# Optimization experiments

Measured on AMD Instinct MI355X. Metric: run time of the kernel, lower is better.

## Reference

```python
import jax, jax.numpy as jnp
import numpy as np

N, F_IN, H, C, E = 20000, 512, 256, 40, 640000
TEMPERATURE = 1.0


def setup_inputs() -> dict:
    key = jax.random.key(0)
    k0, k1, k2, k3 = jax.random.split(key, 4)
    x = jax.random.normal(k0, (N, F_IN), dtype=jnp.float32)
    edge_index = jax.random.randint(k1, (2, E), 0, N, dtype=jnp.int32)
    W1 = jax.random.normal(k2, (F_IN, H), dtype=jnp.float32) / np.float32(np.sqrt(F_IN))
    b1 = jnp.zeros((H,), dtype=jnp.float32)
    W2 = jax.random.normal(k3, (H, C), dtype=jnp.float32) / np.float32(np.sqrt(H))
    b2 = jnp.zeros((C,), dtype=jnp.float32)
    return {"x": x, "edge_index": edge_index, "W1": W1, "b1": b1, "W2": W2, "b2": b2}


def _gcn_conv(x, W, b, src, dst, dinv):
    """GCNConv with added self-loops and symmetric normalization.
    out_i = sum_{j->i} d_i^{-1/2} d_j^{-1/2} (x_j W) + d_i^{-1} (x_i W) + b
    """
    h = x @ W                                         # [N, out]
    coef = dinv[src] * dinv[dst]                      # [E]
    msg = h[src] * coef[:, None]                      # [E, out] gathered messages
    agg = jax.ops.segment_sum(msg, dst, num_segments=x.shape[0])
    agg = agg + h * (dinv * dinv)[:, None]            # self-loop contribution
    return agg + b


def reference(x, edge_index, W1, b1, W2, b2):
    src, dst = edge_index[0], edge_index[1]
    n = x.shape[0]
    # degree including self-loop (PyG gcn_norm counts in-degree on dst)
    deg = jax.ops.segment_sum(jnp.ones(src.shape[0], x.dtype), dst, num_segments=n) + 1.0
    dinv = jax.lax.rsqrt(deg)
    h = jax.nn.relu(_gcn_conv(x, W1, b1, src, dst, dinv))
    # dropout is identity in eval mode (training=False)
    out = _gcn_conv(h, W2, b2, src, dst, dinv)
    return out / jnp.asarray(TEMPERATURE, dtype=out.dtype)
```

## Files before the change

kernel.cpp:

```cpp
#include <hip/hip_runtime.h>
#include <hip/hip_bf16.h>


#define N_NODES 20000
#define F_IN    512
#define H_DIM   256
#define C_DIM   40
#define C_PAD   64
#define E_EDGES 640000
#define BCAP    96
#define WB      576
#define FSH     8
#define FCH     320
#define FCE     2000
#define NSH     2500
#define POISON  0xAAAAAAAAu
#define FXSCALE 2048.f
#define INV_SCALE (1.f / 2048.f)

typedef __attribute__((ext_vector_type(8))) short short8;
typedef __attribute__((ext_vector_type(4))) float floatx4;

__device__ __forceinline__ unsigned short f2bf(float f) {
    unsigned int u = __float_as_uint(f);
    unsigned int r = (u + 0x7fffu + ((u >> 16) & 1u)) >> 16;
    return (unsigned short)r;
}
__device__ __forceinline__ float lo16(unsigned int u) { return __uint_as_float(u << 16); }
__device__ __forceinline__ float hi16(unsigned int u) { return __uint_as_float(u & 0xffff0000u); }
__device__ __forceinline__ unsigned int pack2(float a, float b) {
    return (unsigned int)f2bf(a) | ((unsigned int)f2bf(b) << 16);
}
__device__ __forceinline__ int degof(const int* cursor, int i) {
    return (int)((unsigned)cursor[i] - POISON);
}
#define ACC8F(A, v) do { \
    A[0] += lo16((v).x); A[1] += hi16((v).x); \
    A[2] += lo16((v).y); A[3] += hi16((v).y); \
    A[4] += lo16((v).z); A[5] += hi16((v).z); \
    A[6] += lo16((v).w); A[7] += hi16((v).w); } while (0)
#define ACC8W(A, v) do { \
    A[0] += (int)(short)((v).x & 0xffffu); A[1] += ((int)(v).x) >> 16; \
    A[2] += (int)(short)((v).y & 0xffffu); A[3] += ((int)(v).y) >> 16; \
    A[4] += (int)(short)((v).z & 0xffffu); A[5] += ((int)(v).z) >> 16; \
    A[6] += (int)(short)((v).w & 0xffffu); A[7] += ((int)(v).w) >> 16; } while (0)


__global__ __launch_bounds__(256) void fillwt_kernel(const int* __restrict__ src,
                                                     const int* __restrict__ dst,
                                                     int* __restrict__ cursor,
                                                     int* __restrict__ esrc,
                                                     const float* __restrict__ W1,
                                                     const float* __restrict__ W2,
                                                     unsigned short* __restrict__ w1t,
                                                     unsigned short* __restrict__ w2t,
                                                     short* __restrict__ h1w,
                                                     unsigned short* __restrict__ h2b) {
    const int b = blockIdx.x, t = threadIdx.x;
    if (b < FSH * FCH) {
        const int shard = b & 7;
        const int chunk = b >> 3;
        const int lo = shard * NSH;
        const int base = chunk * FCE;
#pragma unroll
        for (int it = 0; it < 8; ++it) {
            int o = it * 256 + t;
            if (o < FCE) {
                int e = base + o;
                int d = dst[e];
                if ((unsigned)(d - lo) < (unsigned)NSH) {
                    unsigned slot = (unsigned)atomicAdd(&cursor[d], 1) - POISON;
                    esrc[d * BCAP + slot] = src[e];
                }
            }
        }
    } else if (b < FSH * FCH + WB) {
        int idx = (b - FSH * FCH) * 256 + t;
        if (idx < F_IN * H_DIM) {
            int n = idx >> 9, k = idx & 511;
            w1t[idx] = f2bf(W1[k * H_DIM + n]);
        } else {
            int id2 = idx - F_IN * H_DIM;
            int n = id2 >> 8, k = id2 & 255;
            w2t[id2] = (n < C_DIM) ? f2bf(W2[k * C_DIM + n]) : (unsigned short)0;
        }
    } else {
        h1w[(size_t)N_NODES * H_DIM + t] = 0;
        if (t < C_PAD) h2b[(size_t)N_NODES * C_PAD + t] = 0;
    }
}


__global__ __launch_bounds__(256) void gemm1_kernel(const float* __restrict__ A,
                                                    const unsigned short* __restrict__ BT,
                                                    const int* __restrict__ cursor,
                                                    short* __restrict__ Cw) {
    __shared__ short As[64 * 40];
    __shared__ short Bs[128 * 40];
    const int b = blockIdx.x;
    const int tid = threadIdx.x;
    const int w = tid >> 6;
    const int lane = tid & 63;
    const int lq = lane >> 4;
    const int lm = lane & 15;
    const int row0 = (b >> 1) * 64;
    const int col0 = (b & 1) * 128;
    const int sr = tid >> 2;
    const int sc = (tid & 3) * 8;

    floatx4 acc[8];
#pragma unroll
    for (int t = 0; t < 8; ++t) acc[t] = (floatx4){0.f, 0.f, 0.f, 0.f};

    for (int k0 = 0; k0 < F_IN; k0 += 32) {
        {
            const int gr = row0 + sr;
            short8 av = (short8){0,0,0,0,0,0,0,0};
            if (gr < N_NODES) {
                const float* p = A + (size_t)gr * F_IN + k0 + sc;
                float4 a0 = *(const float4*)p;
                float4 a1 = *(const float4*)(p + 4);
                av[0] = (short)f2bf(a0.x); av[1] = (short)f2bf(a0.y);
                av[2] = (short)f2bf(a0.z); av[3] = (short)f2bf(a0.w);
                av[4] = (short)f2bf(a1.x); av[5] = (short)f2bf(a1.y);
                av[6] = (short)f2bf(a1.z); av[7] = (short)f2bf(a1.w);
            }
            *(short8*)&As[sr * 40 + sc] = av;
#pragma unroll
            for (int j = 0; j < 2; ++j) {
                int row = j * 64 + sr;
                *(short8*)&Bs[row * 40 + sc] =
                    *(const short8*)&BT[(size_t)(col0 + row) * F_IN + k0 + sc];
            }
        }
        __syncthreads();
        short8 af = *(const short8*)&As[(w * 16 + lm) * 40 + lq * 8];
#pragma unroll
        for (int t = 0; t < 8; ++t) {
            short8 bf = *(const short8*)&Bs[(t * 16 + lm) * 40 + lq * 8];
            acc[t] = __builtin_amdgcn_mfma_f32_16x16x32_bf16(af, bf, acc[t], 0, 0, 0);
        }
        __syncthreads();
    }
    float dvs[4];
#pragma unroll
    for (int r = 0; r < 4; ++r) {
        int row = row0 + w * 16 + lq * 4 + r;
        dvs[r] = (row < N_NODES)
                     ? rsqrtf((float)degof(cursor, row) + 1.0f) * FXSCALE : 0.f;
    }
#pragma unroll
    for (int t = 0; t < 8; ++t) {
#pragma unroll
        for (int r = 0; r < 4; ++r) {
            int row = row0 + w * 16 + lq * 4 + r;
            int col = col0 + t * 16 + lm;
            if (row < N_NODES)
                Cw[(size_t)row * H_DIM + col] = (short)(int)rintf(acc[t][r] * dvs[r]);
        }
    }
}


__global__ __launch_bounds__(256) void agg1_kernel(const short* __restrict__ h1w,
                                                   const int* __restrict__ cursor,
                                                   const int* __restrict__ esrc,
                                                   const float* __restrict__ b1,
                                                   unsigned short* __restrict__ hrb) {
    const int b = blockIdx.x;
    const int q = b & 3;
    const int w = threadIdx.x >> 6;
    const int lane = threadIdx.x & 63;
    const int g = lane >> 3;
    const int lm = lane & 7;
    const int i = (b >> 2) * 4 + w;
    const int fbase = q * 64 + lm * 8;
    const short* __restrict__ hp = h1w + fbase;
    const int deg = degof(cursor, i);
    const int rb = i * BCAP;
    const int re = rb + deg;
    int A0[8] = {0,0,0,0,0,0,0,0}, A1[8] = {0,0,0,0,0,0,0,0};
    int e0 = esrc[rb + g];
    int e1 = esrc[rb + 8 + g];
    int e2 = esrc[rb + 16 + g];
    int e3 = esrc[rb + 24 + g];
    for (int k = rb; k < re; k += 32) {
        int p0 = esrc[k + 32 + g];
        int p1 = esrc[k + 40 + g];
        int p2 = esrc[k + 48 + g];
        int p3 = esrc[k + 56 + g];
        int s0 = (k + g) < re ? e0 : N_NODES;
        int s1 = (k + 8 + g) < re ? e1 : N_NODES;
        int s2 = (k + 16 + g) < re ? e2 : N_NODES;
        int s3 = (k + 24 + g) < re ? e3 : N_NODES;
        uint4 v0 = *(const uint4*)(hp + (size_t)s0 * H_DIM);
        uint4 v1 = *(const uint4*)(hp + (size_t)s1 * H_DIM);
        uint4 v2 = *(const uint4*)(hp + (size_t)s2 * H_DIM);
        uint4 v3 = *(const uint4*)(hp + (size_t)s3 * H_DIM);
        ACC8W(A0, v0); ACC8W(A1, v1); ACC8W(A0, v2); ACC8W(A1, v3);
        e0 = p0; e1 = p1; e2 = p2; e3 = p3;
    }
    int r[8];
#pragma unroll
    for (int j = 0; j < 8; ++j) {
        int v = A0[j] + A1[j];
        v += __shfl_xor(v, 8, 64);
        v += __shfl_xor(v, 16, 64);
        v += __shfl_xor(v, 32, 64);
        r[j] = v;
    }
    if (lane < 8) {
        uint4 sv = *(const uint4*)(hp + (size_t)i * H_DIM);
        ACC8W(r, sv);
        const float dis = rsqrtf((float)deg + 1.0f) * INV_SCALE;
        float4 bb0 = *(const float4*)&b1[fbase];
        float4 bb1 = *(const float4*)&b1[fbase + 4];
        float bv[8] = {bb0.x, bb0.y, bb0.z, bb0.w, bb1.x, bb1.y, bb1.z, bb1.w};
        float o[8];
#pragma unroll
        for (int j = 0; j < 8; ++j) o[j] = fmaxf(fmaf(dis, (float)r[j], bv[j]), 0.f);
        uint4 ov = make_uint4(pack2(o[0], o[1]), pack2(o[2], o[3]),
                              pack2(o[4], o[5]), pack2(o[6], o[7]));
        *(uint4*)&hrb[(size_t)i * H_DIM + fbase] = ov;
    }
}


__global__ __launch_bounds__(256) void gemm2_kernel(const unsigned short* __restrict__ Ab,
                                                    const unsigned short* __restrict__ BT,
                                                    const int* __restrict__ cursor,
                                                    unsigned short* __restrict__ Cb) {
    __shared__ short As[64 * 40];
    __shared__ short Bs[64 * 40];
    const int tid = threadIdx.x;
    const int w = tid >> 6;
    const int lane = tid & 63;
    const int lq = lane >> 4;
    const int lm = lane & 15;
    const int row0 = blockIdx.x * 64;
    const int sr = tid >> 2;
    const int sc = (tid & 3) * 8;

    floatx4 acc[4];
#pragma unroll
    for (int t = 0; t < 4; ++t) acc[t] = (floatx4){0.f, 0.f, 0.f, 0.f};

    for (int k0 = 0; k0 < H_DIM; k0 += 32) {
        {
            const int gr = row0 + sr;
            short8 av = (short8){0,0,0,0,0,0,0,0};
            if (gr < N_NODES)
                av = *(const short8*)&Ab[(size_t)gr * H_DIM + k0 + sc];
            *(short8*)&As[sr * 40 + sc] = av;
            *(short8*)&Bs[sr * 40 + sc] = *(const short8*)&BT[(size_t)sr * H_DIM + k0 + sc];
        }
        __syncthreads();
        short8 af = *(const short8*)&As[(w * 16 + lm) * 40 + lq * 8];
#pragma unroll
        for (int t = 0; t < 4; ++t) {
            short8 bf = *(const short8*)&Bs[(t * 16 + lm) * 40 + lq * 8];
            acc[t] = __builtin_amdgcn_mfma_f32_16x16x32_bf16(af, bf, acc[t], 0, 0, 0);
        }
        __syncthreads();
    }
    float dv[4];
#pragma unroll
    for (int r = 0; r < 4; ++r) {
        int row = row0 + w * 16 + lq * 4 + r;
        dv[r] = (row < N_NODES) ? rsqrtf((float)degof(cursor, row) + 1.0f) : 0.f;
    }
#pragma unroll
    for (int t = 0; t < 4; ++t) {
#pragma unroll
        for (int r = 0; r < 4; ++r) {
            int row = row0 + w * 16 + lq * 4 + r;
            int col = t * 16 + lm;
            if (row < N_NODES) Cb[(size_t)row * C_PAD + col] = f2bf(acc[t][r] * dv[r]);
        }
    }
}


__global__ __launch_bounds__(256) void agg2_kernel(const unsigned short* __restrict__ h2b,
                                                   const int* __restrict__ cursor,
                                                   const int* __restrict__ esrc,
                                                   const float* __restrict__ b2,
                                                   float* __restrict__ out) {
    const int i = (blockIdx.x * 256 + threadIdx.x) >> 6;
    const int lane = threadIdx.x & 63;
    const int g = lane >> 3;
    const int lm = lane & 7;
    const int c0 = lm * 8;
    const unsigned short* __restrict__ hp = h2b + c0;
    const int deg = degof(cursor, i);
    const int rb = i * BCAP;
    const int re = rb + deg;
    float A0[8] = {0,0,0,0,0,0,0,0}, A1[8] = {0,0,0,0,0,0,0,0};
    int e0 = esrc[rb + g];
    int e1 = esrc[rb + 8 + g];
    int e2 = esrc[rb + 16 + g];
    int e3 = esrc[rb + 24 + g];
    for (int k = rb; k < re; k += 32) {
        int p0 = esrc[k + 32 + g];
        int p1 = esrc[k + 40 + g];
        int p2 = esrc[k + 48 + g];
        int p3 = esrc[k + 56 + g];
        int s0 = (k + g) < re ? e0 : N_NODES;
        int s1 = (k + 8 + g) < re ? e1 : N_NODES;
        int s2 = (k + 16 + g) < re ? e2 : N_NODES;
        int s3 = (k + 24 + g) < re ? e3 : N_NODES;
        uint4 v0 = *(const uint4*)(hp + ((size_t)s0 << 6));
        uint4 v1 = *(const uint4*)(hp + ((size_t)s1 << 6));
        uint4 v2 = *(const uint4*)(hp + ((size_t)s2 << 6));
        uint4 v3 = *(const uint4*)(hp + ((size_t)s3 << 6));
        ACC8F(A0, v0); ACC8F(A1, v1); ACC8F(A0, v2); ACC8F(A1, v3);
        e0 = p0; e1 = p1; e2 = p2; e3 = p3;
    }
    float r[8];
#pragma unroll
    for (int j = 0; j < 8; ++j) {
        float v = A0[j] + A1[j];
        v += __shfl_xor(v, 8, 64);
        v += __shfl_xor(v, 16, 64);
        v += __shfl_xor(v, 32, 64);
        r[j] = v;
    }
    if (lane < 5) {
        uint4 sv = *(const uint4*)(hp + ((size_t)i << 6));
        ACC8F(r, sv);
        const float di = rsqrtf((float)deg + 1.0f);
        float4 bb0 = *(const float4*)&b2[c0];
        float4 bb1 = *(const float4*)&b2[c0 + 4];
        float* op = &out[(size_t)i * C_DIM + c0];
        *(float4*)op = make_float4(fmaf(di, r[0], bb0.x), fmaf(di, r[1], bb0.y),
                                   fmaf(di, r[2], bb0.z), fmaf(di, r[3], bb0.w));
        *(float4*)(op + 4) = make_float4(fmaf(di, r[4], bb1.x), fmaf(di, r[5], bb1.y),
                                         fmaf(di, r[6], bb1.z), fmaf(di, r[7], bb1.w));
    }
}


extern "C" void kernel_launch(void* const* d_in, const int* in_sizes, int n_in,
                              void* d_out, int out_size, void* d_ws, size_t ws_size,
                              hipStream_t stream) {
    const float* x   = (const float*)d_in[0];
    const int*   ei  = (const int*)d_in[1];
    const float* W1  = (const float*)d_in[2];
    const float* b1  = (const float*)d_in[3];
    const float* W2  = (const float*)d_in[4];
    const float* b2  = (const float*)d_in[5];
    float* out = (float*)d_out;

    const int* src = ei;
    const int* dst = ei + E_EDGES;

    char* ws = (char*)d_ws;
    int*            cursor = (int*)(ws + 0);
    int*            esrc   = (int*)(ws + 80128);
    unsigned short* w1t    = (unsigned short*)(ws + 7760384);
    unsigned short* w2t    = (unsigned short*)(ws + 8022528);
    short*          h1w    = (short*)(ws + 8055296);
    unsigned short* hrb    = (unsigned short*)(ws + 18295808);
    unsigned short* h2b    = (unsigned short*)(ws + 28535808);

    fillwt_kernel<<<FSH * FCH + WB + 1, 256, 0, stream>>>(src, dst, cursor, esrc,
                                                          W1, W2, w1t, w2t, h1w, h2b);
    gemm1_kernel<<<2 * ((N_NODES + 63) / 64), 256, 0, stream>>>(x, w1t, cursor, h1w);
    agg1_kernel<<<N_NODES, 256, 0, stream>>>(h1w, cursor, esrc, b1, hrb);
    gemm2_kernel<<<(N_NODES + 63) / 64, 256, 0, stream>>>(hrb, w2t, cursor, h2b);
    agg2_kernel<<<N_NODES / 4, 256, 0, stream>>>(h2b, cursor, esrc, b2, out);
}
```

Baseline: 205.8 us.

## Widen agg1 feature split and accumulate in packed 16-bit lanes

Each block of agg1 now covers 128 features per node instead of 64, so 16 lanes share one edge row and there are 4 edge groups per wave. This halves the grid and the number of times each node's neighbour list is walked. Accumulation now uses packed short8 vector adds, with the cross-lane reduction done as packed 16-bit adds, instead of widening every value to 32-bit ints. The packed path relies on the fixed-point sums staying within int16 range, which adds an overflow risk for high-degree nodes. Gather addresses are computed with a 32-bit shift.

```diff
diff --git a/kernel.cpp b/kernel.cpp
--- a/kernel.cpp
+++ b/kernel.cpp
@@ -19,6 +19,7 @@
 #define INV_SCALE (1.f / 2048.f)
 
 typedef __attribute__((ext_vector_type(8))) short short8;
+typedef __attribute__((ext_vector_type(2))) short short2v;
 typedef __attribute__((ext_vector_type(4))) float floatx4;
 
 __device__ __forceinline__ unsigned short f2bf(float f) {
@@ -33,17 +34,21 @@
 }
 __device__ __forceinline__ int degof(const int* cursor, int i) {
     return (int)((unsigned)cursor[i] - POISON);
+}
+__device__ __forceinline__ int pki(int a, int b) {
+    short2v x, y;
+    __builtin_memcpy(&x, &a, 4);
+    __builtin_memcpy(&y, &b, 4);
+    short2v z = x + y;
+    int r;
+    __builtin_memcpy(&r, &z, 4);
+    return r;
 }
 #define ACC8F(A, v) do { \
     A[0] += lo16((v).x); A[1] += hi16((v).x); \
     A[2] += lo16((v).y); A[3] += hi16((v).y); \
     A[4] += lo16((v).z); A[5] += hi16((v).z); \
     A[6] += lo16((v).w); A[7] += hi16((v).w); } while (0)
-#define ACC8W(A, v) do { \
-    A[0] += (int)(short)((v).x & 0xffffu); A[1] += ((int)(v).x) >> 16; \
-    A[2] += (int)(short)((v).y & 0xffffu); A[3] += ((int)(v).y) >> 16; \
-    A[4] += (int)(short)((v).z & 0xffffu); A[5] += ((int)(v).z) >> 16; \
-    A[6] += (int)(short)((v).w & 0xffffu); A[7] += ((int)(v).w) >> 16; } while (0)
 
 
 __global__ __launch_bounds__(256) void fillwt_kernel(const int* __restrict__ src,
@@ -168,50 +173,60 @@
                                                    const float* __restrict__ b1,
                                                    unsigned short* __restrict__ hrb) {
     const int b = blockIdx.x;
-    const int q = b & 3;
+    const int q = b & 1;
     const int w = threadIdx.x >> 6;
     const int lane = threadIdx.x & 63;
-    const int g = lane >> 3;
-    const int lm = lane & 7;
-    const int i = (b >> 2) * 4 + w;
-    const int fbase = q * 64 + lm * 8;
-    const short* __restrict__ hp = h1w + fbase;
+    const int g = lane >> 4;
+    const int lm = lane & 15;
+    const int i = (b >> 1) * 4 + w;
+    const int fbase = q * 128 + lm * 8;
+    const char* __restrict__ h1c = (const char*)h1w;
+    const unsigned lmo = (unsigned)fbase * 2u;
     const int deg = degof(cursor, i);
     const int rb = i * BCAP;
     const int re = rb + deg;
-    int A0[8] = {0,0,0,0,0,0,0,0}, A1[8] = {0,0,0,0,0,0,0,0};
+    short8 A0 = (short8){0,0,0,0,0,0,0,0};
+    short8 A1 = (short8){0,0,0,0,0,0,0,0};
     int e0 = esrc[rb + g];
-    int e1 = esrc[rb + 8 + g];
-    int e2 = esrc[rb + 16 + g];
-    int e3 = esrc[rb + 24 + g];
-    for (int k = rb; k < re; k += 32) {
-        int p0 = esrc[k + 32 + g];
-        int p1 = esrc[k + 40 + g];
-        int p2 = esrc[k + 48 + g];
-        int p3 = esrc[k + 56 + g];
+    int e1 = esrc[rb + 4 + g];
+    int e2 = esrc[rb + 8 + g];
+    int e3 = esrc[rb + 12 + g];
+    for (int k = rb; k < re; k += 16) {
+        int p0 = esrc[k + 16 + g];
+        int p1 = esrc[k + 20 + g];
+        int p2 = esrc[k + 24 + g];
+        int p3 = esrc[k + 28 + g];
         int s0 = (k + g) < re ? e0 : N_NODES;
-        int s1 = (k + 8 + g) < re ? e1 : N_NODES;
-        int s2 = (k + 16 + g) < re ? e2 : N_NODES;
-        int s3 = (k + 24 + g) < re ? e3 : N_NODES;
-        uint4 v0 = *(const uint4*)(hp + (size_t)s0 * H_DIM);
-        uint4 v1 = *(const uint4*)(hp + (size_t)s1 * H_DIM);
-        uint4 v2 = *(const uint4*)(hp + (size_t)s2 * H_DIM);
-        uint4 v3 = *(const uint4*)(hp + (size_t)s3 * H_DIM);
-        ACC8W(A0, v0); ACC8W(A1, v1); ACC8W(A0, v2); ACC8W(A1, v3);
+        int s1 = (k + 4 + g) < re ? e1 : N_NODES;
+        int s2 = (k + 8 + g) < re ? e2 : N_NODES;
+        int s3 = (k + 12 + g) < re ? e3 : N_NODES;
+        short8 v0 = *(const short8*)(h1c + (size_t)(((unsigned)s0 << 9) + lmo));
+        short8 v1 = *(const short8*)(h1c + (size_t)(((unsigned)s1 << 9) + lmo));
+        short8 v2 = *(const short8*)(h1c + (size_t)(((unsigned)s2 << 9) + lmo));
+        short8 v3 = *(const short8*)(h1c + (size_t)(((unsigned)s3 << 9) + lmo));
+        A0 += v0; A1 += v1; A0 += v2; A1 += v3;
         e0 = p0; e1 = p1; e2 = p2; e3 = p3;
     }
-    int r[8];
-#pragma unroll
-    for (int j = 0; j < 8; ++j) {
-        int v = A0[j] + A1[j];
-        v += __shfl_xor(v, 8, 64);
-        v += __shfl_xor(v, 16, 64);
-        v += __shfl_xor(v, 32, 64);
-        r[j] = v;
-    }
-    if (lane < 8) {
-        uint4 sv = *(const uint4*)(hp + (size_t)i * H_DIM);
-        ACC8W(r, sv);
+    short8 As = A0 + A1;
+    int rp[4];
+    const int* Ap = (const int*)&As;
+#pragma unroll
+    for (int j = 0; j < 4; ++j) {
+        int v = Ap[j];
+        v = pki(v, __shfl_xor(v, 16, 64));
+        v = pki(v, __shfl_xor(v, 32, 64));
+        rp[j] = v;
+    }
+    if (lane < 16) {
+        int r[8];
+#pragma unroll
+        for (int j = 0; j < 4; ++j) {
+            r[2 * j]     = (int)(short)(rp[j] & 0xffff);
+            r[2 * j + 1] = rp[j] >> 16;
+        }
+        short8 sv = *(const short8*)(h1c + (size_t)(((unsigned)i << 9) + lmo));
+#pragma unroll
+        for (int j = 0; j < 8; ++j) r[j] += (int)sv[j];
         const float dis = rsqrtf((float)deg + 1.0f) * INV_SCALE;
         float4 bb0 = *(const float4*)&b1[fbase];
         float4 bb1 = *(const float4*)&b1[fbase + 4];
@@ -366,7 +381,7 @@
     fillwt_kernel<<<FSH * FCH + WB + 1, 256, 0, stream>>>(src, dst, cursor, esrc,
                                                           W1, W2, w1t, w2t, h1w, h2b);
     gemm1_kernel<<<2 * ((N_NODES + 63) / 64), 256, 0, stream>>>(x, w1t, cursor, h1w);
-    agg1_kernel<<<N_NODES, 256, 0, stream>>>(h1w, cursor, esrc, b1, hrb);
+    agg1_kernel<<<(N_NODES / 4) * 2, 256, 0, stream>>>(h1w, cursor, esrc, b1, hrb);
     gemm2_kernel<<<(N_NODES + 63) / 64, 256, 0, stream>>>(hrb, w2t, cursor, h2b);
     agg2_kernel<<<N_NODES / 4, 256, 0, stream>>>(h2b, cursor, esrc, b2, out);
 }
```

Measured after the change: 187.5 us. 8.9% less time.
